# Kernel tuning notes

Measured on AMD Instinct MI355X. Metric: run time of the kernel, lower is better.

## Reference

```python
import jax, jax.numpy as jnp
import numpy as np

B, S, D_MODEL, D_K, D_V = 8, 2048, 1024, 1024, 1024


def setup_inputs() -> dict:
    key = jax.random.key(0)
    k1, k2, k3, k4 = jax.random.split(key, 4)
    x = jax.random.normal(k1, (B, S, D_MODEL), dtype=jnp.float32)
    # Store projection weights as [d_model, d_out] so projection is x @ W
    # (equivalent to torch Linear(d_model, d_out, bias=False) with W^T).
    scale = 1.0 / np.sqrt(D_MODEL)
    Wq = jax.random.normal(k2, (D_MODEL, D_K), dtype=jnp.float32) * scale
    Wk = jax.random.normal(k3, (D_MODEL, D_K), dtype=jnp.float32) * scale
    Wv = jax.random.normal(k4, (D_MODEL, D_V), dtype=jnp.float32) * scale
    return {"x": x, "Wq": Wq, "Wk": Wk, "Wv": Wv}


def reference(x, Wq, Wk, Wv):
    # Single-head causal self-attention, faithful to the original:
    # NOTE: the original scales by sqrt(x.shape[-1]) == sqrt(d_model),
    # not sqrt(d_k of the projection).
    Q = jnp.einsum('bsd,dk->bsk', x, Wq)
    K = jnp.einsum('bsd,dk->bsk', x, Wk)
    V = jnp.einsum('bsd,dv->bsv', x, Wv)
    inv_scale = 1.0 / jnp.sqrt(jnp.asarray(x.shape[-1], x.dtype))
    A = jnp.einsum('bqk,bsk->bqs', Q, K) * inv_scale  # [B, S, S]
    S_len = A.shape[-1]
    causal = jnp.tril(jnp.ones((S_len, S_len), dtype=bool))  # [S, S]
    A = jnp.where(causal, A, -jnp.inf)
    P = jax.nn.softmax(A, axis=-1)
    return jnp.einsum('bqs,bsv->bqv', P, V)
```

## Files before the change

kernel.cpp:

```cpp
#include <hip/hip_runtime.h>
#include <hip/hip_bf16.h>
#include <stdint.h>


typedef __bf16 bf16_t;
typedef __bf16 bf16x4 __attribute__((ext_vector_type(4)));
typedef __bf16 bf16x8 __attribute__((ext_vector_type(8)));
typedef float  floatx4 __attribute__((ext_vector_type(4)));

#define NB 8
#define SS 2048
#define DD 1024
#define INV_SCALE 0.03125f

__device__ __forceinline__ void async_ld16(const void* g, void* l) {
  __builtin_amdgcn_global_load_lds(
      (const __attribute__((address_space(1))) void*)g,
      (__attribute__((address_space(3))) void*)l, 16, 0, 0);
}

__device__ __forceinline__ void mm_core(const bf16_t* __restrict__ Ab,
                                        const bf16_t* __restrict__ Bb,
                                        int lda, int ldb, int kTiles,
                                        bf16_t* sA, bf16_t* sB,
                                        floatx4 acc[4][4]) {
  const int t    = threadIdx.x;
  const int lane = t & 63;
  const int wm   = (t >> 6) >> 1;
  const int wn   = (t >> 6) & 1;
  const int fm   = lane & 15;
  const int q    = lane >> 4;
  const int xo   = fm & 7;

  const bf16_t* ga[4]; const bf16_t* gb[4];
  bf16_t* la[4]; bf16_t* lb[4];
#pragma unroll
  for (int k = 0; k < 4; ++k) {
    const int u   = k * 256 + t;
    const int row = u >> 3;
    const int cc  = (u & 7) ^ (row & 7);
    ga[k] = Ab + (size_t)row * lda + cc * 8;
    gb[k] = Bb + (size_t)row * ldb + cc * 8;
    la[k] = sA + u * 8;
    lb[k] = sB + u * 8;
  }

  const bf16_t* pa = sA + (wm * 64 + fm) * 64;
  const bf16_t* pb = sB + (wn * 64 + fm) * 64;

  for (int kt = 0; kt < kTiles; ++kt) {
    const int ko = kt * 64;
#pragma unroll
    for (int k = 0; k < 4; ++k) async_ld16(ga[k] + ko, la[k]);
#pragma unroll
    for (int k = 0; k < 4; ++k) async_ld16(gb[k] + ko, lb[k]);
    __syncthreads();
#pragma unroll
    for (int h = 0; h < 2; ++h) {
      const int co = ((h * 4 + q) ^ xo) * 8;
      bf16x8 af[4], bfr[4];
#pragma unroll
      for (int i = 0; i < 4; ++i) af[i]  = *(const bf16x8*)(pa + i * 1024 + co);
#pragma unroll
      for (int j = 0; j < 4; ++j) bfr[j] = *(const bf16x8*)(pb + j * 1024 + co);
#pragma unroll
      for (int i = 0; i < 4; ++i)
#pragma unroll
        for (int j = 0; j < 4; ++j)
          acc[i][j] = __builtin_amdgcn_mfma_f32_16x16x32_bf16(bfr[j], af[i], acc[i][j], 0, 0, 0);
    }
    __syncthreads();
  }
}

__device__ __forceinline__ void zero_acc(floatx4 acc[4][4]) {
#pragma unroll
  for (int i = 0; i < 4; ++i)
#pragma unroll
    for (int j = 0; j < 4; ++j)
      acc[i][j] = floatx4{0.f, 0.f, 0.f, 0.f};
}


__global__ __launch_bounds__(256) void prep(const float* __restrict__ x,
                                            const float* __restrict__ Wq,
                                            const float* __restrict__ Wk,
                                            const float* __restrict__ Wv,
                                            bf16_t* __restrict__ xb,
                                            bf16_t* __restrict__ Wt) {
  __shared__ float tile[32][33];
  const int bid = blockIdx.x;
  const int t = threadIdx.x;
  if (bid < 16384) {
    size_t i = (size_t)bid * 256 + t;
    float4 v = ((const float4*)x)[i];
    bf16x4 o = {(bf16_t)v.x, (bf16_t)v.y, (bf16_t)v.z, (bf16_t)v.w};
    ((bf16x4*)xb)[i] = o;
  } else {
    const int wb = bid - 16384;
    const int z = wb >> 10;
    const int rem = wb & 1023;
    const float* W = (z == 0) ? Wq : (z == 1 ? Wk : Wv);
    bf16_t* O = Wt + (size_t)z * DD * DD;
    const int ty = t >> 3;
    const int tx = t & 7;
    const int k0 = (rem >> 5) * 32, n0 = (rem & 31) * 32;
    float4 v = *(const float4*)(W + (size_t)(k0 + ty) * DD + n0 + tx * 4);
    tile[ty][tx * 4 + 0] = v.x;
    tile[ty][tx * 4 + 1] = v.y;
    tile[ty][tx * 4 + 2] = v.z;
    tile[ty][tx * 4 + 3] = v.w;
    __syncthreads();
    bf16x4 o = {(bf16_t)tile[tx * 4 + 0][ty], (bf16_t)tile[tx * 4 + 1][ty],
                (bf16_t)tile[tx * 4 + 2][ty], (bf16_t)tile[tx * 4 + 3][ty]};
    *(bf16x4*)(O + (size_t)(n0 + ty) * DD + k0 + tx * 4) = o;
  }
}


__global__ __launch_bounds__(256) void qkproj_gemm(
    const bf16_t* __restrict__ xb, const bf16_t* __restrict__ Wt,
    bf16_t* __restrict__ QKb) {
  __shared__ __attribute__((aligned(16))) bf16_t sA[128 * 64];
  __shared__ __attribute__((aligned(16))) bf16_t sB[128 * 64];
  const int mt = blockIdx.x, nt = blockIdx.y;
  const bf16_t* Ab = xb + (size_t)mt * 128 * DD;
  const bf16_t* Bb = Wt + (size_t)nt * 128 * DD;
  bf16_t* Cb = QKb + (size_t)mt * 128 * (2 * DD) + nt * 128;
  floatx4 acc[4][4];
  zero_acc(acc);
  mm_core(Ab, Bb, DD, DD, DD / 64, sA, sB, acc);
  const int lane = threadIdx.x & 63;
  const int wm = (threadIdx.x >> 6) >> 1, wn = (threadIdx.x >> 6) & 1;
  const int m0 = wm * 64 + (lane & 15);
  const int n0 = wn * 64 + (lane >> 4) * 4;
#pragma unroll
  for (int i = 0; i < 4; ++i)
#pragma unroll
    for (int j = 0; j < 4; ++j) {
      floatx4 a = acc[i][j];
      bf16x4 o = {(bf16_t)a[0], (bf16_t)a[1], (bf16_t)a[2], (bf16_t)a[3]};
      *(bf16x4*)(Cb + (size_t)(m0 + i * 16) * (2 * DD) + n0 + j * 16) = o;
    }
}


__global__ __launch_bounds__(256) void vproj_gemm(
    const bf16_t* __restrict__ xb, const bf16_t* __restrict__ Wt,
    bf16_t* __restrict__ VtB) {
  __shared__ __attribute__((aligned(16))) bf16_t sA[128 * 64];
  __shared__ __attribute__((aligned(16))) bf16_t sB[128 * 64];
  const int bid = blockIdx.x;
  const int nb = bid & 127;
  const int m  = bid >> 7;
  const int n  = nb & 15;
  const int b  = nb >> 4;
  const bf16_t* Ab = Wt + (size_t)2 * DD * DD + (size_t)m * 128 * DD;
  const bf16_t* Bb = xb + (size_t)b * SS * DD + (size_t)n * 128 * DD;
  bf16_t* Cb = VtB + (size_t)b * DD * SS + (size_t)m * 128 * SS + n * 128;
  floatx4 acc[4][4];
  zero_acc(acc);
  mm_core(Ab, Bb, DD, DD, DD / 64, sA, sB, acc);
  const int lane = threadIdx.x & 63;
  const int wm = (threadIdx.x >> 6) >> 1, wn = (threadIdx.x >> 6) & 1;
  const int m0 = wm * 64 + (lane & 15);
  const int n0 = wn * 64 + (lane >> 4) * 4;
#pragma unroll
  for (int i = 0; i < 4; ++i)
#pragma unroll
    for (int j = 0; j < 4; ++j) {
      floatx4 a = acc[i][j];
      bf16x4 o = {(bf16_t)a[0], (bf16_t)a[1], (bf16_t)a[2], (bf16_t)a[3]};
      *(bf16x4*)(Cb + (size_t)(m0 + i * 16) * SS + n0 + j * 16) = o;
    }
}


__global__ __launch_bounds__(256) void qk_p(
    const bf16_t* __restrict__ Q, const bf16_t* __restrict__ K,
    bf16_t* __restrict__ P, float* __restrict__ lpart) {
  const int b  = blockIdx.x & 7;
  const int tt = 135 - (blockIdx.x >> 3);
  int qi = (int)((sqrtf(8.0f * tt + 1.0f) - 1.0f) * 0.5f);
  while ((qi + 1) * (qi + 2) / 2 <= tt) ++qi;
  while (qi * (qi + 1) / 2 > tt) --qi;
  const int ki = tt - qi * (qi + 1) / 2;

  __shared__ __attribute__((aligned(16))) bf16_t sA[128 * 64];
  __shared__ __attribute__((aligned(16))) bf16_t sB[128 * 64];
  __shared__ float reds[2][128];
  const bf16_t* Ab = Q + ((size_t)b * SS + qi * 128) * (size_t)(2 * DD);
  const bf16_t* Bb = K + ((size_t)b * SS + ki * 128) * (size_t)(2 * DD);
  floatx4 acc[4][4];
  zero_acc(acc);
  mm_core(Ab, Bb, 2 * DD, 2 * DD, DD / 64, sA, sB, acc);

  const int lane = threadIdx.x & 63;
  const int wm = (threadIdx.x >> 6) >> 1, wn = (threadIdx.x >> 6) & 1;
  const bool diag = (ki == qi);
  bf16_t* Pb = P + (size_t)b * SS * SS;
  const int qloc0 = wm * 64 + (lane & 15);
  const int kvb0  = wn * 64 + (lane >> 4) * 4;

#pragma unroll
  for (int i = 0; i < 4; ++i) {
    const int qrow = qloc0 + i * 16;
    float partial = 0.f;
#pragma unroll
    for (int j = 0; j < 4; ++j) {
      const int kvb = kvb0 + j * 16;
      floatx4 p;
#pragma unroll
      for (int r = 0; r < 4; ++r) {
        const float s = acc[i][j][r] * INV_SCALE;
        p[r] = (diag && (kvb + r) > qrow) ? 0.f : __expf(s);
        partial += p[r];
      }
      bf16x4 o = {(bf16_t)p[0], (bf16_t)p[1], (bf16_t)p[2], (bf16_t)p[3]};
      *(bf16x4*)(Pb + (size_t)(qi * 128 + qrow) * SS + ki * 128 + kvb) = o;
    }
    partial += __shfl_xor(partial, 16);
    partial += __shfl_xor(partial, 32);
    if ((lane >> 4) == 0) reds[wn][qrow] = partial;
  }
  __syncthreads();
  const int t = threadIdx.x;
  if (t < 128) {
    size_t row = (size_t)b * SS + qi * 128 + t;
    lpart[row * 16 + ki] = reds[0][t] + reds[1][t];
  }
}


__global__ __launch_bounds__(256) void pv_gemm(
    const bf16_t* __restrict__ P, const bf16_t* __restrict__ Vt,
    const float* __restrict__ lpart, float* __restrict__ Out) {
  const int bid = blockIdx.x;
  const int b  = bid & 7;
  const int nj = (bid >> 3) & 7;
  const int qi = 15 - (bid >> 6);

  __shared__ __attribute__((aligned(16))) bf16_t sA[128 * 64];
  __shared__ __attribute__((aligned(16))) bf16_t sB[128 * 64];
  __shared__ float sRl[128];
  const int t = threadIdx.x;
  if (t < 128) {
    const float* lp = lpart + ((size_t)b * SS + qi * 128 + t) * 16;
    float L = 0.f;
    for (int ci = 0; ci <= qi; ++ci) L += lp[ci];
    sRl[t] = 1.0f / L;
  }
  const bf16_t* Ab = P + (size_t)b * SS * SS + (size_t)qi * 128 * SS;
  const bf16_t* Bb = Vt + (size_t)b * DD * SS + (size_t)nj * 128 * SS;
  float* Cb = Out + (size_t)b * SS * DD + (size_t)qi * 128 * DD + nj * 128;
  floatx4 acc[4][4];
  zero_acc(acc);
  mm_core(Ab, Bb, SS, SS, (qi + 1) * 2, sA, sB, acc);
  const int lane = threadIdx.x & 63;
  const int wm = (threadIdx.x >> 6) >> 1, wn = (threadIdx.x >> 6) & 1;
  const int m0 = wm * 64 + (lane & 15);
  const int n0 = wn * 64 + (lane >> 4) * 4;
#pragma unroll
  for (int i2 = 0; i2 < 4; ++i2) {
    const float scale = sRl[m0 + i2 * 16];
    float* crow = Cb + (size_t)(m0 + i2 * 16) * DD + n0;
#pragma unroll
    for (int j = 0; j < 4; ++j) {
      floatx4 o = acc[i2][j];
      o[0] *= scale; o[1] *= scale; o[2] *= scale; o[3] *= scale;
      *(floatx4*)(crow + j * 16) = o;
    }
  }
}


extern "C" void kernel_launch(void* const* d_in, const int* in_sizes, int n_in,
                              void* d_out, int out_size, void* d_ws, size_t ws_size,
                              hipStream_t stream) {
  const float* x  = (const float*)d_in[0];
  const float* Wq = (const float*)d_in[1];
  const float* Wk = (const float*)d_in[2];
  const float* Wv = (const float*)d_in[3];
  float* out = (float*)d_out;

  char* ws = (char*)d_ws;
  bf16_t* xb   = (bf16_t*)(ws);
  bf16_t* Wt   = (bf16_t*)(ws + 33554432ull);
  bf16_t* QKb  = (bf16_t*)(ws + 39845888ull);
  bf16_t* VtB  = (bf16_t*)(ws + 106954752ull);
  bf16_t* Pb   = (bf16_t*)(ws + 140509184ull);
  float*  lpart= (float*)(ws + 207618048ull);
  (void)in_sizes; (void)n_in; (void)out_size; (void)ws_size;

  prep<<<16384 + 3072, 256, 0, stream>>>(x, Wq, Wk, Wv, xb, Wt);
  qkproj_gemm<<<dim3(128, 16), 256, 0, stream>>>(xb, Wt, QKb);
  vproj_gemm<<<1024, 256, 0, stream>>>(xb, Wt, VtB);
  qk_p<<<1088, 256, 0, stream>>>(QKb, QKb + DD, Pb, lpart);
  pv_gemm<<<1024, 256, 0, stream>>>(Pb, VtB, lpart, out);
}
```

Before: 369.3 us.

## Enlarge GEMM tiles to 256x128 and switch to 32x32x16 MFMA

Every GEMM kernel (both projections, QK^T with softmax numerators, and PV) now uses 256x128 output tiles. Each wave computes a 128x64 sub-tile with 32x32x16 bf16 MFMA instructions instead of 16x16x32. The goal is more arithmetic per LDS and global byte loaded and fewer, larger MFMA issues. In exchange, grids shrink to roughly half as many blocks, LDS per block grows, and the causal triangle is tiled more coarsely (256-row Q blocks against 128-column K blocks), which may waste some masked work and hurt load balance.

```diff
diff --git a/kernel.cpp b/kernel.cpp
--- a/kernel.cpp
+++ b/kernel.cpp
@@ -6,7 +6,8 @@
 typedef __bf16 bf16_t;
 typedef __bf16 bf16x4 __attribute__((ext_vector_type(4)));
 typedef __bf16 bf16x8 __attribute__((ext_vector_type(8)));
-typedef float  floatx4 __attribute__((ext_vector_type(4)));
+typedef float  floatx4  __attribute__((ext_vector_type(4)));
+typedef float  floatx16 __attribute__((ext_vector_type(16)));
 
 #define NB 8
 #define SS 2048
@@ -23,62 +24,65 @@
                                         const bf16_t* __restrict__ Bb,
                                         int lda, int ldb, int kTiles,
                                         bf16_t* sA, bf16_t* sB,
-                                        floatx4 acc[4][4]) {
+                                        floatx16 acc[4][2]) {
   const int t    = threadIdx.x;
   const int lane = t & 63;
   const int wm   = (t >> 6) >> 1;
   const int wn   = (t >> 6) & 1;
-  const int fm   = lane & 15;
-  const int q    = lane >> 4;
+  const int fm   = lane & 31;
+  const int half = lane >> 5;
   const int xo   = fm & 7;
 
-  const bf16_t* ga[4]; const bf16_t* gb[4];
-  bf16_t* la[4]; bf16_t* lb[4];
+  const bf16_t* ga[8]; bf16_t* la[8];
+  const bf16_t* gb[4]; bf16_t* lb[4];
+#pragma unroll
+  for (int k = 0; k < 8; ++k) {
+    const int u = k * 256 + t, row = u >> 3, cc = (u & 7) ^ (row & 7);
+    ga[k] = Ab + (size_t)row * lda + cc * 8;
+    la[k] = sA + u * 8;
+  }
 #pragma unroll
   for (int k = 0; k < 4; ++k) {
-    const int u   = k * 256 + t;
-    const int row = u >> 3;
-    const int cc  = (u & 7) ^ (row & 7);
-    ga[k] = Ab + (size_t)row * lda + cc * 8;
+    const int u = k * 256 + t, row = u >> 3, cc = (u & 7) ^ (row & 7);
     gb[k] = Bb + (size_t)row * ldb + cc * 8;
-    la[k] = sA + u * 8;
     lb[k] = sB + u * 8;
   }
 
-  const bf16_t* pa = sA + (wm * 64 + fm) * 64;
-  const bf16_t* pb = sB + (wn * 64 + fm) * 64;
+  const bf16_t* pa = sA + (size_t)(wm * 128 + fm) * 64;
+  const bf16_t* pb = sB + (size_t)(wn * 64 + fm) * 64;
 
   for (int kt = 0; kt < kTiles; ++kt) {
     const int ko = kt * 64;
 #pragma unroll
-    for (int k = 0; k < 4; ++k) async_ld16(ga[k] + ko, la[k]);
+    for (int k = 0; k < 8; ++k) async_ld16(ga[k] + ko, la[k]);
 #pragma unroll
     for (int k = 0; k < 4; ++k) async_ld16(gb[k] + ko, lb[k]);
     __syncthreads();
 #pragma unroll
-    for (int h = 0; h < 2; ++h) {
-      const int co = ((h * 4 + q) ^ xo) * 8;
-      bf16x8 af[4], bfr[4];
-#pragma unroll
-      for (int i = 0; i < 4; ++i) af[i]  = *(const bf16x8*)(pa + i * 1024 + co);
-#pragma unroll
-      for (int j = 0; j < 4; ++j) bfr[j] = *(const bf16x8*)(pb + j * 1024 + co);
+    for (int s = 0; s < 4; ++s) {
+      const int co = (((2 * s + half)) ^ xo) * 8;
+      bf16x8 af[4], bfr[2];
+#pragma unroll
+      for (int i = 0; i < 4; ++i) af[i]  = *(const bf16x8*)(pa + i * 2048 + co);
+#pragma unroll
+      for (int j = 0; j < 2; ++j) bfr[j] = *(const bf16x8*)(pb + j * 2048 + co);
 #pragma unroll
       for (int i = 0; i < 4; ++i)
 #pragma unroll
-        for (int j = 0; j < 4; ++j)
-          acc[i][j] = __builtin_amdgcn_mfma_f32_16x16x32_bf16(bfr[j], af[i], acc[i][j], 0, 0, 0);
+        for (int j = 0; j < 2; ++j)
+          acc[i][j] = __builtin_amdgcn_mfma_f32_32x32x16_bf16(bfr[j], af[i], acc[i][j], 0, 0, 0);
     }
     __syncthreads();
   }
 }
 
-__device__ __forceinline__ void zero_acc(floatx4 acc[4][4]) {
+__device__ __forceinline__ void zero_acc(floatx16 acc[4][2]) {
 #pragma unroll
   for (int i = 0; i < 4; ++i)
 #pragma unroll
-    for (int j = 0; j < 4; ++j)
-      acc[i][j] = floatx4{0.f, 0.f, 0.f, 0.f};
+    for (int j = 0; j < 2; ++j)
+#pragma unroll
+      for (int r = 0; r < 16; ++r) acc[i][j][r] = 0.f;
 }
 
 
@@ -118,158 +122,162 @@
 }
 
 
-__global__ __launch_bounds__(256) void qkproj_gemm(
+__device__ __forceinline__ void store_c_bf16(floatx16 acc[4][2], bf16_t* Cb, int ldc) {
+  const int lane = threadIdx.x & 63;
+  const int wm = (threadIdx.x >> 6) >> 1, wn = (threadIdx.x >> 6) & 1;
+  const int m0 = wm * 128 + (lane & 31);
+  const int n0 = wn * 64 + (lane >> 5) * 4;
+#pragma unroll
+  for (int i = 0; i < 4; ++i) {
+    bf16_t* crow = Cb + (size_t)(m0 + i * 32) * ldc;
+#pragma unroll
+    for (int j = 0; j < 2; ++j)
+#pragma unroll
+      for (int g = 0; g < 4; ++g) {
+        bf16x4 o = {(bf16_t)acc[i][j][4 * g + 0], (bf16_t)acc[i][j][4 * g + 1],
+                    (bf16_t)acc[i][j][4 * g + 2], (bf16_t)acc[i][j][4 * g + 3]};
+        *(bf16x4*)(crow + n0 + j * 32 + g * 8) = o;
+      }
+  }
+}
+
+
+__global__ __launch_bounds__(256, 2) void qkproj_gemm(
     const bf16_t* __restrict__ xb, const bf16_t* __restrict__ Wt,
     bf16_t* __restrict__ QKb) {
-  __shared__ __attribute__((aligned(16))) bf16_t sA[128 * 64];
+  __shared__ __attribute__((aligned(16))) bf16_t sA[256 * 64];
   __shared__ __attribute__((aligned(16))) bf16_t sB[128 * 64];
   const int mt = blockIdx.x, nt = blockIdx.y;
-  const bf16_t* Ab = xb + (size_t)mt * 128 * DD;
-  const bf16_t* Bb = Wt + (size_t)nt * 128 * DD;
-  bf16_t* Cb = QKb + (size_t)mt * 128 * (2 * DD) + nt * 128;
-  floatx4 acc[4][4];
+  floatx16 acc[4][2];
   zero_acc(acc);
-  mm_core(Ab, Bb, DD, DD, DD / 64, sA, sB, acc);
-  const int lane = threadIdx.x & 63;
-  const int wm = (threadIdx.x >> 6) >> 1, wn = (threadIdx.x >> 6) & 1;
-  const int m0 = wm * 64 + (lane & 15);
-  const int n0 = wn * 64 + (lane >> 4) * 4;
-#pragma unroll
-  for (int i = 0; i < 4; ++i)
-#pragma unroll
-    for (int j = 0; j < 4; ++j) {
-      floatx4 a = acc[i][j];
-      bf16x4 o = {(bf16_t)a[0], (bf16_t)a[1], (bf16_t)a[2], (bf16_t)a[3]};
-      *(bf16x4*)(Cb + (size_t)(m0 + i * 16) * (2 * DD) + n0 + j * 16) = o;
-    }
-}
-
-
-__global__ __launch_bounds__(256) void vproj_gemm(
+  mm_core(xb + (size_t)mt * 256 * DD, Wt + (size_t)nt * 128 * DD,
+          DD, DD, DD / 64, sA, sB, acc);
+  store_c_bf16(acc, QKb + (size_t)mt * 256 * (2 * DD) + nt * 128, 2 * DD);
+}
+
+
+__global__ __launch_bounds__(256, 2) void vproj_gemm(
     const bf16_t* __restrict__ xb, const bf16_t* __restrict__ Wt,
     bf16_t* __restrict__ VtB) {
-  __shared__ __attribute__((aligned(16))) bf16_t sA[128 * 64];
+  __shared__ __attribute__((aligned(16))) bf16_t sA[256 * 64];
   __shared__ __attribute__((aligned(16))) bf16_t sB[128 * 64];
   const int bid = blockIdx.x;
   const int nb = bid & 127;
   const int m  = bid >> 7;
   const int n  = nb & 15;
   const int b  = nb >> 4;
-  const bf16_t* Ab = Wt + (size_t)2 * DD * DD + (size_t)m * 128 * DD;
-  const bf16_t* Bb = xb + (size_t)b * SS * DD + (size_t)n * 128 * DD;
-  bf16_t* Cb = VtB + (size_t)b * DD * SS + (size_t)m * 128 * SS + n * 128;
-  floatx4 acc[4][4];
+  floatx16 acc[4][2];
   zero_acc(acc);
-  mm_core(Ab, Bb, DD, DD, DD / 64, sA, sB, acc);
-  const int lane = threadIdx.x & 63;
-  const int wm = (threadIdx.x >> 6) >> 1, wn = (threadIdx.x >> 6) & 1;
-  const int m0 = wm * 64 + (lane & 15);
-  const int n0 = wn * 64 + (lane >> 4) * 4;
-#pragma unroll
-  for (int i = 0; i < 4; ++i)
-#pragma unroll
-    for (int j = 0; j < 4; ++j) {
-      floatx4 a = acc[i][j];
-      bf16x4 o = {(bf16_t)a[0], (bf16_t)a[1], (bf16_t)a[2], (bf16_t)a[3]};
-      *(bf16x4*)(Cb + (size_t)(m0 + i * 16) * SS + n0 + j * 16) = o;
-    }
-}
-
-
-__global__ __launch_bounds__(256) void qk_p(
+  mm_core(Wt + (size_t)2 * DD * DD + (size_t)m * 256 * DD,
+          xb + (size_t)b * SS * DD + (size_t)n * 128 * DD,
+          DD, DD, DD / 64, sA, sB, acc);
+  store_c_bf16(acc, VtB + (size_t)b * DD * SS + (size_t)m * 256 * SS + n * 128, SS);
+}
+
+
+__global__ __launch_bounds__(256, 2) void qk_p(
     const bf16_t* __restrict__ Q, const bf16_t* __restrict__ K,
     bf16_t* __restrict__ P, float* __restrict__ lpart) {
   const int b  = blockIdx.x & 7;
-  const int tt = 135 - (blockIdx.x >> 3);
-  int qi = (int)((sqrtf(8.0f * tt + 1.0f) - 1.0f) * 0.5f);
-  while ((qi + 1) * (qi + 2) / 2 <= tt) ++qi;
-  while (qi * (qi + 1) / 2 > tt) --qi;
-  const int ki = tt - qi * (qi + 1) / 2;
-
-  __shared__ __attribute__((aligned(16))) bf16_t sA[128 * 64];
+  const int tt = blockIdx.x >> 3;
+  int qi = (int)((sqrtf(4.0f * tt + 1.0f) - 1.0f) * 0.5f);
+  while ((qi + 1) * (qi + 2) <= tt) ++qi;
+  while (qi * (qi + 1) > tt) --qi;
+  const int ki = tt - qi * (qi + 1);
+
+  __shared__ __attribute__((aligned(16))) bf16_t sA[256 * 64];
   __shared__ __attribute__((aligned(16))) bf16_t sB[128 * 64];
-  __shared__ float reds[2][128];
-  const bf16_t* Ab = Q + ((size_t)b * SS + qi * 128) * (size_t)(2 * DD);
-  const bf16_t* Bb = K + ((size_t)b * SS + ki * 128) * (size_t)(2 * DD);
-  floatx4 acc[4][4];
+  __shared__ float reds[2][256];
+  floatx16 acc[4][2];
   zero_acc(acc);
-  mm_core(Ab, Bb, 2 * DD, 2 * DD, DD / 64, sA, sB, acc);
+  mm_core(Q + ((size_t)b * SS + qi * 256) * (2 * DD),
+          K + ((size_t)b * SS + ki * 128) * (2 * DD),
+          2 * DD, 2 * DD, DD / 64, sA, sB, acc);
 
   const int lane = threadIdx.x & 63;
   const int wm = (threadIdx.x >> 6) >> 1, wn = (threadIdx.x >> 6) & 1;
-  const bool diag = (ki == qi);
+  const int m0 = wm * 128 + (lane & 31);
+  const int n0 = wn * 64 + (lane >> 5) * 4;
+  const int diffk = ki * 128 - qi * 256;
   bf16_t* Pb = P + (size_t)b * SS * SS;
-  const int qloc0 = wm * 64 + (lane & 15);
-  const int kvb0  = wn * 64 + (lane >> 4) * 4;
 
 #pragma unroll
   for (int i = 0; i < 4; ++i) {
-    const int qrow = qloc0 + i * 16;
+    const int m = m0 + i * 32;
     float partial = 0.f;
-#pragma unroll
-    for (int j = 0; j < 4; ++j) {
-      const int kvb = kvb0 + j * 16;
-      floatx4 p;
-#pragma unroll
-      for (int r = 0; r < 4; ++r) {
-        const float s = acc[i][j][r] * INV_SCALE;
-        p[r] = (diag && (kvb + r) > qrow) ? 0.f : __expf(s);
-        partial += p[r];
+    bf16_t* prow = Pb + (size_t)(qi * 256 + m) * SS + ki * 128;
+#pragma unroll
+    for (int j = 0; j < 2; ++j)
+#pragma unroll
+      for (int g = 0; g < 4; ++g) {
+        const int nb0 = n0 + j * 32 + g * 8;
+        floatx4 p;
+#pragma unroll
+        for (int r = 0; r < 4; ++r) {
+          const float s = acc[i][j][4 * g + r] * INV_SCALE;
+          p[r] = ((nb0 + r + diffk) > m) ? 0.f : __expf(s);
+          partial += p[r];
+        }
+        bf16x4 o = {(bf16_t)p[0], (bf16_t)p[1], (bf16_t)p[2], (bf16_t)p[3]};
+        *(bf16x4*)(prow + nb0) = o;
       }
-      bf16x4 o = {(bf16_t)p[0], (bf16_t)p[1], (bf16_t)p[2], (bf16_t)p[3]};
-      *(bf16x4*)(Pb + (size_t)(qi * 128 + qrow) * SS + ki * 128 + kvb) = o;
-    }
-    partial += __shfl_xor(partial, 16);
     partial += __shfl_xor(partial, 32);
-    if ((lane >> 4) == 0) reds[wn][qrow] = partial;
+    if (lane < 32) reds[wn][m] = partial;
   }
   __syncthreads();
   const int t = threadIdx.x;
-  if (t < 128) {
-    size_t row = (size_t)b * SS + qi * 128 + t;
+  {
+    size_t row = (size_t)b * SS + qi * 256 + t;
     lpart[row * 16 + ki] = reds[0][t] + reds[1][t];
   }
 }
 
 
-__global__ __launch_bounds__(256) void pv_gemm(
+__global__ __launch_bounds__(256, 2) void pv_gemm(
     const bf16_t* __restrict__ P, const bf16_t* __restrict__ Vt,
     const float* __restrict__ lpart, float* __restrict__ Out) {
   const int bid = blockIdx.x;
+  const int g  = bid >> 6;
+  const int qi = (g < 4) ? (7 - g) : (g - 4);
+  const int nj = (bid >> 3) & 7;
   const int b  = bid & 7;
-  const int nj = (bid >> 3) & 7;
-  const int qi = 15 - (bid >> 6);
-
-  __shared__ __attribute__((aligned(16))) bf16_t sA[128 * 64];
+
+  __shared__ __attribute__((aligned(16))) bf16_t sA[256 * 64];
   __shared__ __attribute__((aligned(16))) bf16_t sB[128 * 64];
-  __shared__ float sRl[128];
+  __shared__ float sRl[256];
   const int t = threadIdx.x;
-  if (t < 128) {
-    const float* lp = lpart + ((size_t)b * SS + qi * 128 + t) * 16;
+  {
+    const float* lp = lpart + ((size_t)b * SS + qi * 256 + t) * 16;
     float L = 0.f;
-    for (int ci = 0; ci <= qi; ++ci) L += lp[ci];
+    const int nch = 2 * qi + 2;
+    for (int ci = 0; ci < nch; ++ci) L += lp[ci];
     sRl[t] = 1.0f / L;
   }
-  const bf16_t* Ab = P + (size_t)b * SS * SS + (size_t)qi * 128 * SS;
-  const bf16_t* Bb = Vt + (size_t)b * DD * SS + (size_t)nj * 128 * SS;
-  float* Cb = Out + (size_t)b * SS * DD + (size_t)qi * 128 * DD + nj * 128;
-  floatx4 acc[4][4];
+  floatx16 acc[4][2];
   zero_acc(acc);
-  mm_core(Ab, Bb, SS, SS, (qi + 1) * 2, sA, sB, acc);
+  mm_core(P + (size_t)b * SS * SS + (size_t)qi * 256 * SS,
+          Vt + (size_t)b * DD * SS + (size_t)nj * 128 * SS,
+          SS, SS, (qi + 1) * 4, sA, sB, acc);
+
   const int lane = threadIdx.x & 63;
   const int wm = (threadIdx.x >> 6) >> 1, wn = (threadIdx.x >> 6) & 1;
-  const int m0 = wm * 64 + (lane & 15);
-  const int n0 = wn * 64 + (lane >> 4) * 4;
-#pragma unroll
-  for (int i2 = 0; i2 < 4; ++i2) {
-    const float scale = sRl[m0 + i2 * 16];
-    float* crow = Cb + (size_t)(m0 + i2 * 16) * DD + n0;
-#pragma unroll
-    for (int j = 0; j < 4; ++j) {
-      floatx4 o = acc[i2][j];
-      o[0] *= scale; o[1] *= scale; o[2] *= scale; o[3] *= scale;
-      *(floatx4*)(crow + j * 16) = o;
-    }
+  const int m0 = wm * 128 + (lane & 31);
+  const int n0 = wn * 64 + (lane >> 5) * 4;
+  float* Cb = Out + (size_t)b * SS * DD + (size_t)qi * 256 * DD + nj * 128;
+#pragma unroll
+  for (int i = 0; i < 4; ++i) {
+    const int m = m0 + i * 32;
+    const float scale = sRl[m];
+    float* crow = Cb + (size_t)m * DD;
+#pragma unroll
+    for (int j = 0; j < 2; ++j)
+#pragma unroll
+      for (int g2 = 0; g2 < 4; ++g2) {
+        floatx4 o;
+#pragma unroll
+        for (int r = 0; r < 4; ++r) o[r] = acc[i][j][4 * g2 + r] * scale;
+        *(floatx4*)(crow + n0 + j * 32 + g2 * 8) = o;
+      }
   }
 }
 
@@ -293,8 +301,8 @@
   (void)in_sizes; (void)n_in; (void)out_size; (void)ws_size;
 
   prep<<<16384 + 3072, 256, 0, stream>>>(x, Wq, Wk, Wv, xb, Wt);
-  qkproj_gemm<<<dim3(128, 16), 256, 0, stream>>>(xb, Wt, QKb);
-  vproj_gemm<<<1024, 256, 0, stream>>>(xb, Wt, VtB);
-  qk_p<<<1088, 256, 0, stream>>>(QKb, QKb + DD, Pb, lpart);
-  pv_gemm<<<1024, 256, 0, stream>>>(Pb, VtB, lpart, out);
-}
+  qkproj_gemm<<<dim3(64, 16), 256, 0, stream>>>(xb, Wt, QKb);
+  vproj_gemm<<<512, 256, 0, stream>>>(xb, Wt, VtB);
+  qk_p<<<576, 256, 0, stream>>>(QKb, QKb + DD, Pb, lpart);
+  pv_gemm<<<512, 256, 0, stream>>>(Pb, VtB, lpart, out);
+}
```

Measured after the change: 376.5 us. About the same (+2.0%).
